# Optimization experiments

Measured on AMD Instinct MI355X. Metric: run time of the kernel, lower is better.

## Reference

```python
import jax, jax.numpy as jnp
import numpy as np


def _lstm_layer(x, Wih, Whh, bih, bhh):
    # x: (B, S, I); Wih: (4H, I); Whh: (4H, H)
    B, S, _ = x.shape
    H = Whh.shape[1]
    # Big batched GEMM for all input projections at once.
    xproj = jnp.einsum('bsi,gi->bsg', x, Wih) + bih + bhh  # (B, S, 4H)
    xproj_t = jnp.transpose(xproj, (1, 0, 2))              # (S, B, 4H)

    def step(carry, xp):
        h, c = carry
        gates = xp + h @ Whh.T                             # (B, 4H)
        i, f, g, o = jnp.split(gates, 4, axis=-1)          # torch gate order i,f,g,o
        i = jax.nn.sigmoid(i)
        f = jax.nn.sigmoid(f)
        g = jnp.tanh(g)
        o = jax.nn.sigmoid(o)
        c = f * c + i * g
        h = o * jnp.tanh(c)
        return (h, c), h

    h0 = jnp.zeros((B, H), dtype=x.dtype)
    c0 = jnp.zeros((B, H), dtype=x.dtype)
    (_, _), hs = jax.lax.scan(step, (h0, c0), xproj_t)     # hs: (S, B, H)
    return jnp.transpose(hs, (1, 0, 2))                    # (B, S, H)


def setup_inputs() -> dict:
    key = jax.random.key(0)
    ks = jax.random.split(key, 12)
    B, S, I, H, O = 64, 512, 512, 1024, 64
    s_in = 1.0 / np.sqrt(H)
    inp = {
        'x': jax.random.normal(ks[0], (B, S, I), dtype=jnp.float32),
        'Wih0': jax.random.uniform(ks[1], (4 * H, I), minval=-s_in, maxval=s_in),
        'Whh0': jax.random.uniform(ks[2], (4 * H, H), minval=-s_in, maxval=s_in),
        'bih0': jax.random.uniform(ks[3], (4 * H,), minval=-s_in, maxval=s_in),
        'bhh0': jax.random.uniform(ks[4], (4 * H,), minval=-s_in, maxval=s_in),
        'Wih1': jax.random.uniform(ks[5], (4 * H, H), minval=-s_in, maxval=s_in),
        'Whh1': jax.random.uniform(ks[6], (4 * H, H), minval=-s_in, maxval=s_in),
        'bih1': jax.random.uniform(ks[7], (4 * H,), minval=-s_in, maxval=s_in),
        'bhh1': jax.random.uniform(ks[8], (4 * H,), minval=-s_in, maxval=s_in),
        'Wfc': jax.random.uniform(ks[9], (O, H), minval=-s_in, maxval=s_in),
        'bfc': jax.random.uniform(ks[10], (O,), minval=-s_in, maxval=s_in),
    }
    return inp


def reference(x, Wih0, Whh0, bih0, bhh0, Wih1, Whh1, bih1, bhh1, Wfc, bfc):
    h = _lstm_layer(x, Wih0, Whh0, bih0, bhh0)   # (B, S, H)
    h = _lstm_layer(h, Wih1, Whh1, bih1, bhh1)   # (B, S, H)
    # dropout = 0.0 (eval mode) -> identity
    logits = jnp.einsum('bsh,oh->bso', h, Wfc) + bfc  # (B, S, O)
    return logits
```

## Files before the change

kernel.cpp:

```cpp
#include <hip/hip_runtime.h>
#include <stdint.h>

typedef _Float16 f16;
typedef _Float16 f16x8 __attribute__((ext_vector_type(8)));
typedef float f32x4 __attribute__((ext_vector_type(4)));

#define MFMA16(a, b, c) __builtin_amdgcn_mfma_f32_16x16x32_f16((a), (b), (c), 0, 0, 0)



__global__ void k_conv_x(const float* __restrict__ x, f16* __restrict__ x16) {
  int i = blockIdx.x * 256 + threadIdx.x;
  int o = i * 8;
  int s = o >> 15, b = (o >> 9) & 63, c = o & 511;
  const float* src = x + (size_t)b * 262144 + (size_t)s * 512 + c;
  float4 v0 = *(const float4*)(src);
  float4 v1 = *(const float4*)(src + 4);
  union { f16 h[8]; f16x8 v; } t;
  t.h[0] = (f16)v0.x; t.h[1] = (f16)v0.y; t.h[2] = (f16)v0.z; t.h[3] = (f16)v0.w;
  t.h[4] = (f16)v1.x; t.h[5] = (f16)v1.y; t.h[6] = (f16)v1.z; t.h[7] = (f16)v1.w;
  *(f16x8*)(x16 + o) = t.v;
}

__global__ void k_conv_wfrag(const float* __restrict__ Wih, const float* __restrict__ Whh,
                             f16* __restrict__ Wf, int KI, int KK, int kPer) {
  int fid = blockIdx.x;
  int lane = threadIdx.x;
  int cf = fid & 3; int rest = fid >> 2;
  int kk = rest % KK; rest /= KK; int w = rest & 7; int jc = rest >> 3;
  int c = cf * 16 + (lane & 15);
  int g = (c >> 4) * 1024 + jc * 16 + (c & 15);
  int k = w * kPer + kk * 32 + ((lane >> 4) << 3);
  const float* src = (k < KI) ? (Wih + (size_t)g * KI + k)
                              : (Whh + (size_t)g * 1024 + (k - KI));
  union { f16 h[8]; f16x8 v; } t;
#pragma unroll
  for (int i = 0; i < 8; ++i) t.h[i] = (f16)src[i];
  *(f16x8*)(Wf + ((size_t)fid * 64 + lane) * 8) = t.v;
}

__global__ void k_conv_bias(const float* __restrict__ bih, const float* __restrict__ bhh,
                            float* __restrict__ br) {
  int d = blockIdx.x * 64 + threadIdx.x;
  int jc = d >> 6, c = d & 63;
  int g = (c >> 4) * 1024 + jc * 16 + (c & 15);
  br[d] = bih[g] + bhh[g];
}

__global__ void k_conv_wfc(const float* __restrict__ Wfc, f16* __restrict__ Wfc16) {
  int i = blockIdx.x * 256 + threadIdx.x;
  Wfc16[i] = (f16)Wfc[i];
}

__global__ __attribute__((amdgpu_flat_work_group_size(512, 512), amdgpu_waves_per_eu(2, 2)))
void k_persist(const f16* __restrict__ x16,
               const f16* __restrict__ W0f, const float* __restrict__ b0r,
               const f16* __restrict__ W1f, const float* __restrict__ b1r,
               f16* __restrict__ h0buf, f16* __restrict__ h1buf,
               f16* __restrict__ h1all, unsigned char* flags8) {
  const int layer = blockIdx.x >> 7;
  const int sub = blockIdx.x & 127;
  const int rh = sub >> 6, jc = sub & 63;

  __shared__ float cred[8][32][69];

  unsigned char* myflag = flags8 + layer * 128 + sub;

  const int tid = threadIdx.x;
  const int w = tid >> 6, lane = tid & 63;
  const int l15 = lane & 15, q8 = (lane >> 4) << 3;
  const int rbase = rh * 32;
  const int m = tid >> 4, jl = tid & 15;

  const float* bias = (layer ? b1r : b0r) + jc * 64;
  const float bI = bias[jl], bF = bias[16 + jl], bG = bias[32 + jl], bO = bias[48 + jl];
  float creg = 0.f;

#define POLLG(n0v, n1v)                                                                  \
  {                                                                                      \
    if (w == 0) {                                                                        \
      int needI = (lane < 32) ? (n0v) : (n1v);                                           \
      if (needI < 0) needI = 0;                                                          \
      unsigned int nb = (unsigned int)needI & 255u;                                      \
      const unsigned int* fp_ = (const unsigned int*)flags8 + lane;                      \
      for (;;) {                                                                         \
        unsigned int v_;                                                                 \
        asm volatile("global_load_dword %0, %1, off sc0 sc1\n\ts_waitcnt vmcnt(0)"       \
                     : "=&v"(v_) : "v"(fp_) : "memory");                                 \
        unsigned int ok = (((v_ & 255u) - nb) & 255u) < 128u;                            \
        ok &= ((((v_ >> 8) & 255u) - nb) & 255u) < 128u;                                 \
        ok &= ((((v_ >> 16) & 255u) - nb) & 255u) < 128u;                                \
        ok &= ((((v_ >> 24) & 255u) - nb) & 255u) < 128u;                                \
        if (__all(ok)) break;                                                            \
        __builtin_amdgcn_s_sleep(1);                                                     \
      }                                                                                  \
    }                                                                                    \
    __syncthreads();                                                                     \
  }

#define CRED_AND_POINTWISE(HOUT, HALL)                                                   \
  {                                                                                      \
    _Pragma("unroll") for (int rf = 0; rf < 2; ++rf)                                     \
      _Pragma("unroll") for (int cf = 0; cf < 4; ++cf)                                   \
        _Pragma("unroll") for (int r = 0; r < 4; ++r)                                    \
          cred[w][rf * 16 + (lane >> 4) * 4 + r][cf * 16 + l15] = acc[rf][cf][r];        \
    __syncthreads();                                                                     \
    float ip = bI, fp = bF, gp2 = bG, op = bO;                                           \
    _Pragma("unroll") for (int ww = 0; ww < 8; ++ww) {                                   \
      ip += cred[ww][m][jl];                                                             \
      fp += cred[ww][m][16 + jl];                                                        \
      gp2 += cred[ww][m][32 + jl];                                                       \
      op += cred[ww][m][48 + jl];                                                        \
    }                                                                                    \
    float ig = 1.f / (1.f + __expf(-ip));                                                \
    float fg = 1.f / (1.f + __expf(-fp));                                                \
    float ea = __expf(-2.f * fabsf(gp2));                                                \
    float gg = copysignf((1.f - ea) / (1.f + ea), gp2);                                  \
    float og = 1.f / (1.f + __expf(-op));                                                \
    creg = fg * creg + ig * gg;                                                          \
    float eb = __expf(-2.f * fabsf(creg));                                               \
    float hval = og * copysignf((1.f - eb) / (1.f + eb), creg);                          \
    size_t idx = (size_t)(rbase + m) * 1024 + jc * 16 + jl;                              \
    union { f16 h; unsigned short s; } cv; cv.h = (f16)hval;                             \
    __hip_atomic_store((unsigned short*)((HOUT) + idx), cv.s,                            \
                       __ATOMIC_RELAXED, __HIP_MEMORY_SCOPE_AGENT);                      \
    if (HALL) ((f16*)(HALL))[idx] = cv.h;                                                \
    __syncthreads();                          \
    if (tid == 0) {                                                                      \
      unsigned int fv = (unsigned int)(t + 1) & 255u;                                    \
      asm volatile("global_store_byte %0, %1, off sc0 sc1" ::                            \
                   "v"(myflag), "v"(fv) : "memory");                                     \
    }                                                                                    \
  }

#define GLD_X(dst, addr)                                                                 \
  asm volatile("global_load_dwordx4 %0, %1, off sc0 sc1" : "=&v"(dst) : "v"(addr) : "memory")
#define GLD_C(dst, addr)                                                                 \
  asm volatile("global_load_dwordx4 %0, %1, off" : "=&v"(dst) : "v"(addr) : "memory")
#define WAITV(n)                                                                         \
  { asm volatile("s_waitcnt vmcnt(" #n ")" ::: "memory"); __builtin_amdgcn_sched_barrier(0); }

  if (layer == 0) {
    const int KK = 6;
    f16x8 wreg[6][4];
#pragma unroll
    for (int kk = 0; kk < KK; ++kk)
#pragma unroll
      for (int cf = 0; cf < 4; ++cf)
        wreg[kk][cf] = *(const f16x8*)(W0f + ((size_t)((jc * 8 + w) * KK + kk) * 4 + cf) * 512 + lane * 8);
#pragma unroll
    for (int kk = 0; kk < KK; ++kk)
      asm volatile("" : "+v"(wreg[kk][0]), "+v"(wreg[kk][1]), "+v"(wreg[kk][2]), "+v"(wreg[kk][3]));

    const int kbeg = w * 192;
    for (int t = 0; t < 512; ++t) {
      const f16* A0x = x16 + (size_t)t * 32768;
      const f16* A1h = h0buf + (size_t)((t + 3) & 3) * 65536;
      f16* hout = h0buf + (size_t)(t & 3) * 65536;

      f16x8 af[4][2];
#define ISSUE0(kk)                                                                       \
      {                                                                                  \
        int k_ = kbeg + (kk) * 32 + q8;                                                  \
        if (k_ < 512) {                                                                  \
          const f16* ap_ = A0x + k_;                                                     \
          GLD_C(af[(kk) & 3][0], ap_ + (size_t)(rbase + l15) * 512);                     \
          GLD_C(af[(kk) & 3][1], ap_ + (size_t)(rbase + 16 + l15) * 512);                \
        } else {                                                                         \
          const f16* ap_ = A1h + (k_ - 512);                                             \
          GLD_X(af[(kk) & 3][0], ap_ + (size_t)(rbase + l15) * 1024);                    \
          GLD_X(af[(kk) & 3][1], ap_ + (size_t)(rbase + 16 + l15) * 1024);               \
        }                                                                                \
      }
#define MF0(kk)                                                                          \
      { _Pragma("unroll") for (int rf = 0; rf < 2; ++rf)                                 \
          _Pragma("unroll") for (int cf = 0; cf < 4; ++cf)                               \
            acc[rf][cf] = MFMA16(af[(kk) & 3][rf], wreg[kk][cf], acc[rf][cf]); }

      f32x4 acc[2][4];
#pragma unroll
      for (int i = 0; i < 2; ++i)
#pragma unroll
        for (int j = 0; j < 4; ++j) acc[i][j] = f32x4{0.f, 0.f, 0.f, 0.f};

      if (w <= 2) { ISSUE0(0) ISSUE0(1) ISSUE0(2) ISSUE0(3) }
      POLLG(t, t - 3);
      if (w > 2) { ISSUE0(0) ISSUE0(1) ISSUE0(2) ISSUE0(3) }
      WAITV(6) MF0(0) ISSUE0(4)
      WAITV(6) MF0(1) ISSUE0(5)
      WAITV(6) MF0(2)
      WAITV(4) MF0(3)
      WAITV(2) MF0(4)
      WAITV(0) MF0(5)
#undef ISSUE0
#undef MF0

      CRED_AND_POINTWISE(hout, (f16*)nullptr);
    }
  } else {
    const int KK = 8;
    f16x8 wreg[8][4];
#pragma unroll
    for (int kk = 0; kk < KK; ++kk)
#pragma unroll
      for (int cf = 0; cf < 4; ++cf)
        wreg[kk][cf] = *(const f16x8*)(W1f + ((size_t)((jc * 8 + w) * KK + kk) * 4 + cf) * 512 + lane * 8);
#pragma unroll
    for (int kk = 0; kk < KK; ++kk)
      asm volatile("" : "+v"(wreg[kk][0]), "+v"(wreg[kk][1]), "+v"(wreg[kk][2]), "+v"(wreg[kk][3]));

    const int kbeg = w * 256;
    for (int t = 0; t < 512; ++t) {
      const f16* A0 = h0buf + (size_t)(t & 3) * 65536;
      const f16* A1 = h1buf + (size_t)((t + 3) & 3) * 65536;
      f16* hout = h1buf + (size_t)(t & 3) * 65536;
      f16* hall = h1all + (size_t)t * 65536;

      POLLG(t + 1, t);

      f16x8 af[4][2];
#define ISSUE1(kk)                                                                       \
      {                                                                                  \
        int k_ = kbeg + (kk) * 32 + q8;                                                  \
        const f16* ap_ = (k_ < 1024) ? (A0 + k_) : (A1 + (k_ - 1024));                   \
        GLD_X(af[(kk) & 3][0], ap_ + (size_t)(rbase + l15) * 1024);                      \
        GLD_X(af[(kk) & 3][1], ap_ + (size_t)(rbase + 16 + l15) * 1024);                 \
      }
#define MF1(kk)                                                                          \
      { _Pragma("unroll") for (int rf = 0; rf < 2; ++rf)                                 \
          _Pragma("unroll") for (int cf = 0; cf < 4; ++cf)                               \
            acc[rf][cf] = MFMA16(af[(kk) & 3][rf], wreg[kk][cf], acc[rf][cf]); }

      f32x4 acc[2][4];
#pragma unroll
      for (int i = 0; i < 2; ++i)
#pragma unroll
        for (int j = 0; j < 4; ++j) acc[i][j] = f32x4{0.f, 0.f, 0.f, 0.f};

      ISSUE1(0) ISSUE1(1) ISSUE1(2) ISSUE1(3)
      WAITV(6) MF1(0) ISSUE1(4)
      WAITV(6) MF1(1) ISSUE1(5)
      WAITV(6) MF1(2) ISSUE1(6)
      WAITV(6) MF1(3) ISSUE1(7)
      WAITV(6) MF1(4)
      WAITV(4) MF1(5)
      WAITV(2) MF1(6)
      WAITV(0) MF1(7)
#undef ISSUE1
#undef MF1

      CRED_AND_POINTWISE(hout, hall);
    }
  }
#undef POLLG
#undef CRED_AND_POINTWISE
#undef GLD_X
#undef GLD_C
#undef WAITV
}

__global__ __launch_bounds__(512, 1)
void k_fc(const f16* __restrict__ h1all, const f16* __restrict__ Wfc16,
          const float* __restrict__ bfc, float* __restrict__ out) {
  const int s = blockIdx.x;
  const f16* A = h1all + (size_t)s * 65536;
  __shared__ float credf[8][64][68];

  const int w = threadIdx.x >> 6;
  const int lane = threadIdx.x & 63;
  const int l15 = lane & 15;
  const int ksub = (lane >> 4) << 3;

  f32x4 acc[4][4];
#pragma unroll
  for (int i = 0; i < 4; ++i)
#pragma unroll
    for (int j = 0; j < 4; ++j) acc[i][j] = f32x4{0.f, 0.f, 0.f, 0.f};

  const int kbeg = w * 128, kend = kbeg + 128;
  f16x8 af0[4], bf0[4], af1[4], bf1[4];

  auto LOADK = [&](int kc, f16x8(&a)[4], f16x8(&b)[4]) {
    const f16* ap = A + kc + ksub;
#pragma unroll
    for (int rf = 0; rf < 4; ++rf)
      a[rf] = *(const f16x8*)(ap + (size_t)(rf * 16 + l15) * 1024);
    const f16* bp = Wfc16 + kc + ksub;
#pragma unroll
    for (int cf = 0; cf < 4; ++cf)
      b[cf] = *(const f16x8*)(bp + (size_t)(cf * 16 + l15) * 1024);
  };

  LOADK(kbeg, af0, bf0);
  for (int kc = kbeg; kc < kend; kc += 64) {
    LOADK(kc + 32, af1, bf1);
#pragma unroll
    for (int rf = 0; rf < 4; ++rf)
#pragma unroll
      for (int cf = 0; cf < 4; ++cf) acc[rf][cf] = MFMA16(af0[rf], bf0[cf], acc[rf][cf]);
    if (kc + 64 < kend) LOADK(kc + 64, af0, bf0);
#pragma unroll
    for (int rf = 0; rf < 4; ++rf)
#pragma unroll
      for (int cf = 0; cf < 4; ++cf) acc[rf][cf] = MFMA16(af1[rf], bf1[cf], acc[rf][cf]);
  }

#pragma unroll
  for (int rf = 0; rf < 4; ++rf)
#pragma unroll
    for (int cf = 0; cf < 4; ++cf)
#pragma unroll
      for (int r = 0; r < 4; ++r)
        credf[w][rf * 16 + (lane >> 4) * 4 + r][cf * 16 + l15] = acc[rf][cf][r];

  __syncthreads();

  int m = threadIdx.x >> 3;
  int cbase = (threadIdx.x & 7) * 8;
#pragma unroll
  for (int u = 0; u < 8; ++u) {
    int col = cbase + u;
    float v = bfc[col];
#pragma unroll
    for (int ww = 0; ww < 8; ++ww) v += credf[ww][m][col];
    out[((size_t)m * 512 + s) * 64 + col] = v;
  }
}

extern "C" void kernel_launch(void* const* d_in, const int* in_sizes, int n_in,
                              void* d_out, int out_size, void* d_ws, size_t ws_size,
                              hipStream_t stream) {
  const float* x    = (const float*)d_in[0];
  const float* Wih0 = (const float*)d_in[1];
  const float* Whh0 = (const float*)d_in[2];
  const float* bih0 = (const float*)d_in[3];
  const float* bhh0 = (const float*)d_in[4];
  const float* Wih1 = (const float*)d_in[5];
  const float* Whh1 = (const float*)d_in[6];
  const float* bih1 = (const float*)d_in[7];
  const float* bhh1 = (const float*)d_in[8];
  const float* Wfc  = (const float*)d_in[9];
  const float* bfc  = (const float*)d_in[10];
  float* out = (float*)d_out;

  char* ws = (char*)d_ws;
  f16*   W0f   = (f16*)(ws + 0);
  f16*   W1f   = (f16*)(ws + 12582912);
  f16*   Wfc16 = (f16*)(ws + 29360128);
  float* b0r   = (float*)(ws + 29491200);
  float* b1r   = (float*)(ws + 29507584);
  f16*   x16   = (f16*)(ws + 29523968);
  f16*   h1all = (f16*)(ws + 63078400);
  f16*   h0buf = (f16*)(ws + 130187264);
  f16*   h1buf = (f16*)(ws + 130711552);
  unsigned char* flags8 = (unsigned char*)(ws + 131235840);

  k_conv_x<<<8192, 256, 0, stream>>>(x, x16);
  k_conv_wfrag<<<12288, 64, 0, stream>>>(Wih0, Whh0, W0f, 512, 6, 192);
  k_conv_wfrag<<<16384, 64, 0, stream>>>(Wih1, Whh1, W1f, 1024, 8, 256);
  k_conv_bias<<<64, 64, 0, stream>>>(bih0, bhh0, b0r);
  k_conv_bias<<<64, 64, 0, stream>>>(bih1, bhh1, b1r);
  k_conv_wfc<<<256, 256, 0, stream>>>(Wfc, Wfc16);
  hipMemsetAsync(ws + 130187264, 0, 524288 * 2 + 256, stream);

  {
    const f16* x16c = x16; const f16* W0fc = W0f; const float* b0rc = b0r;
    const f16* W1fc = W1f; const float* b1rc = b1r;
    f16 *p0 = h0buf, *p1 = h1buf, *ph = h1all;
    unsigned char* fl = flags8;
    void* kargs[] = { &x16c, &W0fc, &b0rc, &W1fc, &b1rc, &p0, &p1, &ph, &fl };
    hipLaunchCooperativeKernel((void*)k_persist, dim3(256), dim3(512), kargs, 0, stream);
  }

  k_fc<<<512, 512, 0, stream>>>(h1all, Wfc16, bfc, out);
}
```

Measured before the change: 4.681 ms.

## Use per-wave fine-grained flags and deeper h ring buffers in persistent LSTM kernel

Replaces the block-level flag (one wave polls, then a block barrier) with per-wave flags, so each wave waits only for the hidden-state slice it actually reads. The weight fragments are re-laid out so each wave's K range matches the producing blocks' column chunks. The h ring buffers grow from 4 to 8 slots, which lets the producer fall further behind before it must wait. Layer 1 now issues its own-layer h loads before checking the layer-0 flag, which adds more polling traffic and more complex correctness reasoning in exchange for less serialization.

Result: slower. 12.04 ms (+157.2%).

```diff
diff --git a/kernel.cpp b/kernel.cpp
--- a/kernel.cpp
+++ b/kernel.cpp
@@ -23,14 +23,17 @@
 }
 
 __global__ void k_conv_wfrag(const float* __restrict__ Wih, const float* __restrict__ Whh,
-                             f16* __restrict__ Wf, int KI, int KK, int kPer) {
+                             f16* __restrict__ Wf, int KI, int KK, int mode) {
   int fid = blockIdx.x;
   int lane = threadIdx.x;
   int cf = fid & 3; int rest = fid >> 2;
   int kk = rest % KK; rest /= KK; int w = rest & 7; int jc = rest >> 3;
   int c = cf * 16 + (lane & 15);
   int g = (c >> 4) * 1024 + jc * 16 + (c & 15);
-  int k = w * kPer + kk * 32 + ((lane >> 4) << 3);
+  int k;
+  if (mode == 0) k = (kk < 2) ? (w * 64 + kk * 32) : (512 + w * 128 + (kk - 2) * 32);
+  else           k = (kk < 4) ? (w * 128 + kk * 32) : (1024 + w * 128 + (kk - 4) * 32);
+  k += (lane >> 4) << 3;
   const float* src = (k < KI) ? (Wih + (size_t)g * KI + k)
                               : (Whh + (size_t)g * 1024 + (k - KI));
   union { f16 h[8]; f16x8 v; } t;
@@ -64,41 +67,41 @@
 
   __shared__ float cred[8][32][69];
 
-  unsigned char* myflag = flags8 + layer * 128 + sub;
-
   const int tid = threadIdx.x;
   const int w = tid >> 6, lane = tid & 63;
   const int l15 = lane & 15, q8 = (lane >> 4) << 3;
   const int rbase = rh * 32;
   const int m = tid >> 4, jl = tid & 15;
 
+  const int SET0 = rh * 512;
+  const int SET1 = (2 + rh) * 512;
+  unsigned char* myflag = flags8 + (layer * 2 + rh) * 512 + jc * 8 + w;
+
   const float* bias = (layer ? b1r : b0r) + jc * 64;
   const float bI = bias[jl], bF = bias[16 + jl], bG = bias[32 + jl], bO = bias[48 + jl];
   float creg = 0.f;
 
-#define POLLG(n0v, n1v)                                                                  \
+#define POLLW(SOFF, NEEDV)                                                               \
   {                                                                                      \
-    if (w == 0) {                                                                        \
-      int needI = (lane < 32) ? (n0v) : (n1v);                                           \
-      if (needI < 0) needI = 0;                                                          \
-      unsigned int nb = (unsigned int)needI & 255u;                                      \
-      const unsigned int* fp_ = (const unsigned int*)flags8 + lane;                      \
-      for (;;) {                                                                         \
-        unsigned int v_;                                                                 \
-        asm volatile("global_load_dword %0, %1, off sc0 sc1\n\ts_waitcnt vmcnt(0)"       \
-                     : "=&v"(v_) : "v"(fp_) : "memory");                                 \
-        unsigned int ok = (((v_ & 255u) - nb) & 255u) < 128u;                            \
-        ok &= ((((v_ >> 8) & 255u) - nb) & 255u) < 128u;                                 \
-        ok &= ((((v_ >> 16) & 255u) - nb) & 255u) < 128u;                                \
-        ok &= ((((v_ >> 24) & 255u) - nb) & 255u) < 128u;                                \
-        if (__all(ok)) break;                                                            \
-        __builtin_amdgcn_s_sleep(1);                                                     \
+    int needI = (NEEDV); if (needI < 0) needI = 0;                                       \
+    unsigned int nb = (unsigned int)needI & 255u;                                        \
+    const unsigned long long* fp_ =                                                      \
+        (const unsigned long long*)(flags8 + (SOFF)) + lane;                             \
+    for (;;) {                                                                           \
+      unsigned long long v_;                                                             \
+      asm volatile("global_load_dwordx2 %0, %1, off sc0 sc1\n\ts_waitcnt vmcnt(0)"       \
+                   : "=&v"(v_) : "v"(fp_) : "memory");                                   \
+      unsigned int ok = 1u;                                                              \
+      _Pragma("unroll") for (int b_ = 0; b_ < 8; ++b_) {                                 \
+        unsigned int bv = (unsigned int)(v_ >> (b_ * 8)) & 255u;                         \
+        ok &= (((bv - nb) & 255u) < 128u);                                               \
       }                                                                                  \
+      if (__all(ok)) break;                                                              \
+      __builtin_amdgcn_s_sleep(1);                                                       \
     }                                                                                    \
-    __syncthreads();                                                                     \
-  }
-
-#define CRED_AND_POINTWISE(HOUT, HALL)                                                   \
+  }
+
+#define CRED_AND_POINTWISE(HOUT, HALL, PRESTORE)                                         \
   {                                                                                      \
     _Pragma("unroll") for (int rf = 0; rf < 2; ++rf)                                     \
       _Pragma("unroll") for (int cf = 0; cf < 4; ++cf)                                   \
@@ -120,17 +123,19 @@
     creg = fg * creg + ig * gg;                                                          \
     float eb = __expf(-2.f * fabsf(creg));                                               \
     float hval = og * copysignf((1.f - eb) / (1.f + eb), creg);                          \
+    PRESTORE                                                                             \
     size_t idx = (size_t)(rbase + m) * 1024 + jc * 16 + jl;                              \
     union { f16 h; unsigned short s; } cv; cv.h = (f16)hval;                             \
     __hip_atomic_store((unsigned short*)((HOUT) + idx), cv.s,                            \
                        __ATOMIC_RELAXED, __HIP_MEMORY_SCOPE_AGENT);                      \
     if (HALL) ((f16*)(HALL))[idx] = cv.h;                                                \
-    __syncthreads();                          \
-    if (tid == 0) {                                                                      \
+    asm volatile("s_waitcnt vmcnt(0)" ::: "memory");                                     \
+    if (lane == 0) {                                                                     \
       unsigned int fv = (unsigned int)(t + 1) & 255u;                                    \
       asm volatile("global_store_byte %0, %1, off sc0 sc1" ::                            \
                    "v"(myflag), "v"(fv) : "memory");                                     \
     }                                                                                    \
+    __syncthreads();                            \
   }
 
 #define GLD_X(dst, addr)                                                                 \
@@ -152,30 +157,30 @@
     for (int kk = 0; kk < KK; ++kk)
       asm volatile("" : "+v"(wreg[kk][0]), "+v"(wreg[kk][1]), "+v"(wreg[kk][2]), "+v"(wreg[kk][3]));
 
-    const int kbeg = w * 192;
     for (int t = 0; t < 512; ++t) {
       const f16* A0x = x16 + (size_t)t * 32768;
-      const f16* A1h = h0buf + (size_t)((t + 3) & 3) * 65536;
-      f16* hout = h0buf + (size_t)(t & 3) * 65536;
-
-      f16x8 af[4][2];
-#define ISSUE0(kk)                                                                       \
+      const f16* A1h = h0buf + (size_t)((t + 7) & 7) * 65536;
+      f16* hout = h0buf + (size_t)(t & 7) * 65536;
+
+      f16x8 af[6][2];
+#define ISSUE_X(kk)                                                                      \
       {                                                                                  \
-        int k_ = kbeg + (kk) * 32 + q8;                                                  \
-        if (k_ < 512) {                                                                  \
-          const f16* ap_ = A0x + k_;                                                     \
-          GLD_C(af[(kk) & 3][0], ap_ + (size_t)(rbase + l15) * 512);                     \
-          GLD_C(af[(kk) & 3][1], ap_ + (size_t)(rbase + 16 + l15) * 512);                \
-        } else {                                                                         \
-          const f16* ap_ = A1h + (k_ - 512);                                             \
-          GLD_X(af[(kk) & 3][0], ap_ + (size_t)(rbase + l15) * 1024);                    \
-          GLD_X(af[(kk) & 3][1], ap_ + (size_t)(rbase + 16 + l15) * 1024);               \
-        }                                                                                \
+        int k_ = w * 64 + (kk) * 32 + q8;                                                \
+        const f16* ap_ = A0x + k_;                                                       \
+        GLD_C(af[kk][0], ap_ + (size_t)(rbase + l15) * 512);                             \
+        GLD_C(af[kk][1], ap_ + (size_t)(rbase + 16 + l15) * 512);                        \
+      }
+#define ISSUE_H0(kk)                                                                     \
+      {                                                                                  \
+        int hk_ = w * 128 + ((kk) - 2) * 32 + q8;                                        \
+        const f16* ap_ = A1h + hk_;                                                      \
+        GLD_X(af[kk][0], ap_ + (size_t)(rbase + l15) * 1024);                            \
+        GLD_X(af[kk][1], ap_ + (size_t)(rbase + 16 + l15) * 1024);                       \
       }
 #define MF0(kk)                                                                          \
       { _Pragma("unroll") for (int rf = 0; rf < 2; ++rf)                                 \
           _Pragma("unroll") for (int cf = 0; cf < 4; ++cf)                               \
-            acc[rf][cf] = MFMA16(af[(kk) & 3][rf], wreg[kk][cf], acc[rf][cf]); }
+            acc[rf][cf] = MFMA16(af[kk][rf], wreg[kk][cf], acc[rf][cf]); }
 
       f32x4 acc[2][4];
 #pragma unroll
@@ -183,19 +188,19 @@
 #pragma unroll
         for (int j = 0; j < 4; ++j) acc[i][j] = f32x4{0.f, 0.f, 0.f, 0.f};
 
-      if (w <= 2) { ISSUE0(0) ISSUE0(1) ISSUE0(2) ISSUE0(3) }
-      POLLG(t, t - 3);
-      if (w > 2) { ISSUE0(0) ISSUE0(1) ISSUE0(2) ISSUE0(3) }
-      WAITV(6) MF0(0) ISSUE0(4)
-      WAITV(6) MF0(1) ISSUE0(5)
+      ISSUE_X(0) ISSUE_X(1)
+      POLLW(SET0, t);
+      ISSUE_H0(2) ISSUE_H0(3) ISSUE_H0(4) ISSUE_H0(5)
+      MF0(0) MF0(1)
       WAITV(6) MF0(2)
       WAITV(4) MF0(3)
       WAITV(2) MF0(4)
       WAITV(0) MF0(5)
-#undef ISSUE0
+#undef ISSUE_X
+#undef ISSUE_H0
 #undef MF0
 
-      CRED_AND_POINTWISE(hout, (f16*)nullptr);
+      CRED_AND_POINTWISE(hout, (f16*)nullptr, POLLW(SET1, t - 7);)
     }
   } else {
     const int KK = 8;
@@ -209,27 +214,24 @@
     for (int kk = 0; kk < KK; ++kk)
       asm volatile("" : "+v"(wreg[kk][0]), "+v"(wreg[kk][1]), "+v"(wreg[kk][2]), "+v"(wreg[kk][3]));
 
-    const int kbeg = w * 256;
     for (int t = 0; t < 512; ++t) {
-      const f16* A0 = h0buf + (size_t)(t & 3) * 65536;
-      const f16* A1 = h1buf + (size_t)((t + 3) & 3) * 65536;
-      f16* hout = h1buf + (size_t)(t & 3) * 65536;
+      const f16* A0 = h0buf + (size_t)(t & 7) * 65536;
+      const f16* A1 = h1buf + (size_t)((t + 7) & 7) * 65536;
+      f16* hout = h1buf + (size_t)(t & 7) * 65536;
       f16* hall = h1all + (size_t)t * 65536;
 
-      POLLG(t + 1, t);
-
-      f16x8 af[4][2];
-#define ISSUE1(kk)                                                                       \
+      f16x8 af[8][2];
+#define ISSUE_HH(kk, BASE)                                                               \
       {                                                                                  \
-        int k_ = kbeg + (kk) * 32 + q8;                                                  \
-        const f16* ap_ = (k_ < 1024) ? (A0 + k_) : (A1 + (k_ - 1024));                   \
-        GLD_X(af[(kk) & 3][0], ap_ + (size_t)(rbase + l15) * 1024);                      \
-        GLD_X(af[(kk) & 3][1], ap_ + (size_t)(rbase + 16 + l15) * 1024);                 \
+        int hk_ = w * 128 + ((kk) & 3) * 32 + q8;                                        \
+        const f16* ap_ = (BASE) + hk_;                                                   \
+        GLD_X(af[kk][0], ap_ + (size_t)(rbase + l15) * 1024);                            \
+        GLD_X(af[kk][1], ap_ + (size_t)(rbase + 16 + l15) * 1024);                       \
       }
 #define MF1(kk)                                                                          \
       { _Pragma("unroll") for (int rf = 0; rf < 2; ++rf)                                 \
           _Pragma("unroll") for (int cf = 0; cf < 4; ++cf)                               \
-            acc[rf][cf] = MFMA16(af[(kk) & 3][rf], wreg[kk][cf], acc[rf][cf]); }
+            acc[rf][cf] = MFMA16(af[kk][rf], wreg[kk][cf], acc[rf][cf]); }
 
       f32x4 acc[2][4];
 #pragma unroll
@@ -237,22 +239,24 @@
 #pragma unroll
         for (int j = 0; j < 4; ++j) acc[i][j] = f32x4{0.f, 0.f, 0.f, 0.f};
 
-      ISSUE1(0) ISSUE1(1) ISSUE1(2) ISSUE1(3)
-      WAITV(6) MF1(0) ISSUE1(4)
-      WAITV(6) MF1(1) ISSUE1(5)
-      WAITV(6) MF1(2) ISSUE1(6)
-      WAITV(6) MF1(3) ISSUE1(7)
-      WAITV(6) MF1(4)
-      WAITV(4) MF1(5)
-      WAITV(2) MF1(6)
-      WAITV(0) MF1(7)
-#undef ISSUE1
+      POLLW(SET1, t);
+      ISSUE_HH(4, A1) ISSUE_HH(5, A1) ISSUE_HH(6, A1) ISSUE_HH(7, A1)
+      POLLW(SET0, t + 1);
+      ISSUE_HH(0, A0) ISSUE_HH(1, A0)
+      MF1(4) MF1(5)
+      ISSUE_HH(2, A0) ISSUE_HH(3, A0)
+      MF1(6) MF1(7)
+      WAITV(6) MF1(0)
+      WAITV(4) MF1(1)
+      WAITV(2) MF1(2)
+      WAITV(0) MF1(3)
+#undef ISSUE_HH
 #undef MF1
 
-      CRED_AND_POINTWISE(hout, hall);
+      CRED_AND_POINTWISE(hout, hall, ;)
     }
   }
-#undef POLLG
+#undef POLLW
 #undef CRED_AND_POINTWISE
 #undef GLD_X
 #undef GLD_C
@@ -352,16 +356,16 @@
   f16*   x16   = (f16*)(ws + 29523968);
   f16*   h1all = (f16*)(ws + 63078400);
   f16*   h0buf = (f16*)(ws + 130187264);
-  f16*   h1buf = (f16*)(ws + 130711552);
-  unsigned char* flags8 = (unsigned char*)(ws + 131235840);
+  f16*   h1buf = (f16*)(ws + 131235840);
+  unsigned char* flags8 = (unsigned char*)(ws + 132284416);
 
   k_conv_x<<<8192, 256, 0, stream>>>(x, x16);
-  k_conv_wfrag<<<12288, 64, 0, stream>>>(Wih0, Whh0, W0f, 512, 6, 192);
-  k_conv_wfrag<<<16384, 64, 0, stream>>>(Wih1, Whh1, W1f, 1024, 8, 256);
+  k_conv_wfrag<<<12288, 64, 0, stream>>>(Wih0, Whh0, W0f, 512, 6, 0);
+  k_conv_wfrag<<<16384, 64, 0, stream>>>(Wih1, Whh1, W1f, 1024, 8, 1);
   k_conv_bias<<<64, 64, 0, stream>>>(bih0, bhh0, b0r);
   k_conv_bias<<<64, 64, 0, stream>>>(bih1, bhh1, b1r);
   k_conv_wfc<<<256, 256, 0, stream>>>(Wfc, Wfc16);
-  hipMemsetAsync(ws + 130187264, 0, 524288 * 2 + 256, stream);
+  hipMemsetAsync(ws + 130187264, 0, 1048576 * 2 + 2048, stream);
 
   {
     const f16* x16c = x16; const f16* W0fc = W0f; const float* b0rc = b0r;
```

## Rebalance layer-0 K split so every wave prefetches x before polling

Applied to the files above, without the earlier changes.

Layer 0's K dimension is redistributed so each of the 8 waves handles 64 input columns plus 128 recurrent columns, instead of contiguous 192-column slices. Every wave can now issue its x-projection loads before the cross-block flag poll, and only the h loads wait on it. Flags are regrouped by row-half, so each block polls only the 32 flags of its own batch half. The cred LDS padding also shrinks. The aim is to cut recurrence-critical latency per timestep, at the cost of more h loads issued after the poll in each wave.

Measured after the change: 4.837 ms. 1.03x slower.

```diff
diff --git a/kernel.cpp b/kernel.cpp
--- a/kernel.cpp
+++ b/kernel.cpp
@@ -23,14 +23,17 @@
 }
 
 __global__ void k_conv_wfrag(const float* __restrict__ Wih, const float* __restrict__ Whh,
-                             f16* __restrict__ Wf, int KI, int KK, int kPer) {
+                             f16* __restrict__ Wf, int KI, int KK, int mode) {
   int fid = blockIdx.x;
   int lane = threadIdx.x;
   int cf = fid & 3; int rest = fid >> 2;
   int kk = rest % KK; rest /= KK; int w = rest & 7; int jc = rest >> 3;
   int c = cf * 16 + (lane & 15);
   int g = (c >> 4) * 1024 + jc * 16 + (c & 15);
-  int k = w * kPer + kk * 32 + ((lane >> 4) << 3);
+  int k = (mode == 0)
+              ? ((kk < 2) ? (w * 64 + kk * 32) : (512 + w * 128 + (kk - 2) * 32))
+              : (w * 256 + kk * 32);
+  k += (lane >> 4) << 3;
   const float* src = (k < KI) ? (Wih + (size_t)g * KI + k)
                               : (Whh + (size_t)g * 1024 + (k - KI));
   union { f16 h[8]; f16x8 v; } t;
@@ -62,9 +65,9 @@
   const int sub = blockIdx.x & 127;
   const int rh = sub >> 6, jc = sub & 63;
 
-  __shared__ float cred[8][32][69];
-
-  unsigned char* myflag = flags8 + layer * 128 + sub;
+  __shared__ float cred[8][32][66];
+
+  unsigned char* myflag = flags8 + rh * 128 + layer * 64 + jc;
 
   const int tid = threadIdx.x;
   const int w = tid >> 6, lane = tid & 63;
@@ -79,10 +82,11 @@
 #define POLLG(n0v, n1v)                                                                  \
   {                                                                                      \
     if (w == 0) {                                                                        \
-      int needI = (lane < 32) ? (n0v) : (n1v);                                           \
+      int li = lane & 31;                                                                \
+      int needI = (li < 16) ? (n0v) : (n1v);                                             \
       if (needI < 0) needI = 0;                                                          \
       unsigned int nb = (unsigned int)needI & 255u;                                      \
-      const unsigned int* fp_ = (const unsigned int*)flags8 + lane;                      \
+      const unsigned int* fp_ = (const unsigned int*)(flags8 + rh * 128) + li;           \
       for (;;) {                                                                         \
         unsigned int v_;                                                                 \
         asm volatile("global_load_dword %0, %1, off sc0 sc1\n\ts_waitcnt vmcnt(0)"       \
@@ -125,7 +129,7 @@
     __hip_atomic_store((unsigned short*)((HOUT) + idx), cv.s,                            \
                        __ATOMIC_RELAXED, __HIP_MEMORY_SCOPE_AGENT);                      \
     if (HALL) ((f16*)(HALL))[idx] = cv.h;                                                \
-    __syncthreads();                          \
+    __syncthreads();                   \
     if (tid == 0) {                                                                      \
       unsigned int fv = (unsigned int)(t + 1) & 255u;                                    \
       asm volatile("global_store_byte %0, %1, off sc0 sc1" ::                            \
@@ -152,30 +156,30 @@
     for (int kk = 0; kk < KK; ++kk)
       asm volatile("" : "+v"(wreg[kk][0]), "+v"(wreg[kk][1]), "+v"(wreg[kk][2]), "+v"(wreg[kk][3]));
 
-    const int kbeg = w * 192;
     for (int t = 0; t < 512; ++t) {
       const f16* A0x = x16 + (size_t)t * 32768;
       const f16* A1h = h0buf + (size_t)((t + 3) & 3) * 65536;
       f16* hout = h0buf + (size_t)(t & 3) * 65536;
 
-      f16x8 af[4][2];
-#define ISSUE0(kk)                                                                       \
+      f16x8 af[6][2];
+#define ISSUE_X(kk)                                                                      \
       {                                                                                  \
-        int k_ = kbeg + (kk) * 32 + q8;                                                  \
-        if (k_ < 512) {                                                                  \
-          const f16* ap_ = A0x + k_;                                                     \
-          GLD_C(af[(kk) & 3][0], ap_ + (size_t)(rbase + l15) * 512);                     \
-          GLD_C(af[(kk) & 3][1], ap_ + (size_t)(rbase + 16 + l15) * 512);                \
-        } else {                                                                         \
-          const f16* ap_ = A1h + (k_ - 512);                                             \
-          GLD_X(af[(kk) & 3][0], ap_ + (size_t)(rbase + l15) * 1024);                    \
-          GLD_X(af[(kk) & 3][1], ap_ + (size_t)(rbase + 16 + l15) * 1024);               \
-        }                                                                                \
+        int k_ = w * 64 + (kk) * 32 + q8;                                                \
+        const f16* ap_ = A0x + k_;                                                       \
+        GLD_C(af[kk][0], ap_ + (size_t)(rbase + l15) * 512);                             \
+        GLD_C(af[kk][1], ap_ + (size_t)(rbase + 16 + l15) * 512);                        \
+      }
+#define ISSUE_H0(kk)                                                                     \
+      {                                                                                  \
+        int hk_ = w * 128 + ((kk) - 2) * 32 + q8;                                        \
+        const f16* ap_ = A1h + hk_;                                                      \
+        GLD_X(af[kk][0], ap_ + (size_t)(rbase + l15) * 1024);                            \
+        GLD_X(af[kk][1], ap_ + (size_t)(rbase + 16 + l15) * 1024);                       \
       }
 #define MF0(kk)                                                                          \
       { _Pragma("unroll") for (int rf = 0; rf < 2; ++rf)                                 \
           _Pragma("unroll") for (int cf = 0; cf < 4; ++cf)                               \
-            acc[rf][cf] = MFMA16(af[(kk) & 3][rf], wreg[kk][cf], acc[rf][cf]); }
+            acc[rf][cf] = MFMA16(af[kk][rf], wreg[kk][cf], acc[rf][cf]); }
 
       f32x4 acc[2][4];
 #pragma unroll
@@ -183,16 +187,16 @@
 #pragma unroll
         for (int j = 0; j < 4; ++j) acc[i][j] = f32x4{0.f, 0.f, 0.f, 0.f};
 
-      if (w <= 2) { ISSUE0(0) ISSUE0(1) ISSUE0(2) ISSUE0(3) }
+      ISSUE_X(0) ISSUE_X(1)
       POLLG(t, t - 3);
-      if (w > 2) { ISSUE0(0) ISSUE0(1) ISSUE0(2) ISSUE0(3) }
-      WAITV(6) MF0(0) ISSUE0(4)
-      WAITV(6) MF0(1) ISSUE0(5)
-      WAITV(6) MF0(2)
-      WAITV(4) MF0(3)
-      WAITV(2) MF0(4)
-      WAITV(0) MF0(5)
-#undef ISSUE0
+      ISSUE_H0(2) ISSUE_H0(3) ISSUE_H0(4) ISSUE_H0(5)
+      WAITV(8)  MF0(0) MF0(1)
+      WAITV(6)  MF0(2)
+      WAITV(4)  MF0(3)
+      WAITV(2)  MF0(4)
+      WAITV(0)  MF0(5)
+#undef ISSUE_X
+#undef ISSUE_H0
 #undef MF0
 
       CRED_AND_POINTWISE(hout, (f16*)nullptr);
@@ -356,8 +360,8 @@
   unsigned char* flags8 = (unsigned char*)(ws + 131235840);
 
   k_conv_x<<<8192, 256, 0, stream>>>(x, x16);
-  k_conv_wfrag<<<12288, 64, 0, stream>>>(Wih0, Whh0, W0f, 512, 6, 192);
-  k_conv_wfrag<<<16384, 64, 0, stream>>>(Wih1, Whh1, W1f, 1024, 8, 256);
+  k_conv_wfrag<<<12288, 64, 0, stream>>>(Wih0, Whh0, W0f, 512, 6, 0);
+  k_conv_wfrag<<<16384, 64, 0, stream>>>(Wih1, Whh1, W1f, 1024, 8, 1);
   k_conv_bias<<<64, 64, 0, stream>>>(bih0, bhh0, b0r);
   k_conv_bias<<<64, 64, 0, stream>>>(bih1, bhh1, b1r);
   k_conv_wfc<<<256, 256, 0, stream>>>(Wfc, Wfc16);
```
